# Optimization experiments

Hardware: AMD Instinct MI355X
Metric: run time of the kernel (lower is better)

## Reference

```python
import jax, jax.numpy as jnp
import numpy as np

IN_C = 256
OUT_C = 256
QK_C = OUT_C // 8  # channel_reduction_rate = 8
B, H, W = 8, 64, 64


def setup_inputs() -> dict:
    key = jax.random.key(0)
    ks = jax.random.split(key, 7)
    s_in = 1.0 / np.sqrt(IN_C)  # torch Conv2d default init scale (kernel=1)
    return {
        "x": jax.random.normal(ks[0], (B, IN_C, H, W), dtype=jnp.float32),
        "W1": jax.random.uniform(ks[1], (OUT_C, IN_C), jnp.float32, -s_in, s_in),
        "b1": jax.random.uniform(ks[2], (OUT_C,), jnp.float32, -s_in, s_in),
        "W2": jax.random.uniform(ks[3], (QK_C, IN_C), jnp.float32, -s_in, s_in),
        "b2": jax.random.uniform(ks[4], (QK_C,), jnp.float32, -s_in, s_in),
        "W3": jax.random.uniform(ks[5], (QK_C, IN_C), jnp.float32, -s_in, s_in),
        "b3": jax.random.uniform(ks[6], (QK_C,), jnp.float32, -s_in, s_in),
    }


def reference(x, W1, b1, W2, b2, W3, b3):
    b, c, h, w = x.shape
    n = h * w
    xf = x.reshape(b, c, n)  # 1x1 conv == channel matmul on flattened spatial
    v = jnp.einsum("oc,bcn->bon", W1, xf) + b1[None, :, None]   # [B, OUT_C, N]
    q = jnp.einsum("oc,bcn->bon", W2, xf) + b2[None, :, None]   # [B, QK_C, N]
    k = jnp.einsum("oc,bcn->bon", W3, xf) + b3[None, :, None]   # [B, QK_C, N]
    scores = jnp.einsum("bdn,bdm->bnm", q, k)                    # [B, N, N]
    # GLOBAL softmax over the full flattened NxN matrix per batch element
    attn = jax.nn.softmax(scores.reshape(b, -1), axis=1).reshape(b, n, n)
    out = jnp.einsum("bon,bnm->bom", v, attn)                    # [B, OUT_C, N]
    return out.reshape(x.shape) + x
```

## Files before the change

### kernel.cpp

```cpp
#include <hip/hip_runtime.h>
#include <hip/hip_bf16.h>
#include <math.h>

#define NBATCH 8
#define NC 256
#define ND 32
#define SN 4096

constexpr size_t VB_B   = 0;
constexpr size_t QT_B   = 16777216;
constexpr size_t KT_B   = QT_B + 2097152;
constexpr size_t PM_B   = KT_B + 2097152;
constexpr size_t PS_B   = PM_B + 32768;
constexpr size_t C_B    = PS_B + 32768;
constexpr size_t WB_B   = C_B + 64;
constexpr size_t BIAS_B = WB_B + 163840;
constexpr size_t PB_B   = BIAS_B + 1280;

typedef __attribute__((ext_vector_type(8))) short short8;
typedef __attribute__((ext_vector_type(4))) float f32x4;

__device__ __forceinline__ unsigned bf16rne(float f) {
  unsigned u = __float_as_uint(f);
  return (u + 0x7fffu + ((u >> 16) & 1u)) >> 16;
}
__device__ __forceinline__ unsigned bfpack2(float lo, float hi) {
  union { __hip_bfloat162 h; unsigned u; } cv;
  cv.h.x = __float2bfloat16(lo);
  cv.h.y = __float2bfloat16(hi);
  return cv.u;
}

__global__ __launch_bounds__(256) void prep_kernel(
    const float* __restrict__ W1, const float* __restrict__ b1,
    const float* __restrict__ W2, const float* __restrict__ b2,
    const float* __restrict__ W3, const float* __restrict__ b3,
    char* __restrict__ wsb)
{
  ushort* Wb = (ushort*)(wsb + WB_B);
  float* bias = (float*)(wsb + BIAS_B);
  const float LOG2E = 1.4426950408889634f;
  int idx = blockIdx.x * 256 + threadIdx.x;
  int r = idx >> 6, c4 = (idx & 63) * 4;
  float4 v; float sc = 1.0f;
  if (r < 256)      { v = *(const float4*)(W1 + (size_t)r * 256 + c4); }
  else if (r < 288) { v = *(const float4*)(W2 + (size_t)(r - 256) * 256 + c4); sc = LOG2E; }
  else              { v = *(const float4*)(W3 + (size_t)(r - 288) * 256 + c4); }
  ushort4 o;
  o.x = (ushort)bf16rne(v.x * sc); o.y = (ushort)bf16rne(v.y * sc);
  o.z = (ushort)bf16rne(v.z * sc); o.w = (ushort)bf16rne(v.w * sc);
  *(ushort4*)(Wb + (size_t)r * 256 + c4) = o;
  if (blockIdx.x == 0 && threadIdx.x < 320) {
    int q = threadIdx.x;
    bias[q] = q < 256 ? b1[q] : (q < 288 ? b2[q - 256] * LOG2E : b3[q - 288]);
  }
}

__global__ __launch_bounds__(512) void proj_kernel(
    const float* __restrict__ x, char* __restrict__ wsb)
{
  __shared__ alignas(16) char xT[65536];
  __shared__ alignas(16) char Wsh[40960];
  const int bid = blockIdx.x;
  const int b = bid & 7, nt = bid >> 3;
  const int n0 = nt * 128;
  const int t = threadIdx.x, w = t >> 6, lane = t & 63;
  const int l4 = lane >> 4, l16 = lane & 15;
  const float* xb = x + (size_t)b * NC * SN;
  const ushort* Wb = (const ushort*)(wsb + WB_B);
  const float* bias = (const float*)(wsb + BIAS_B);
  ushort* vbuf  = (ushort*)(wsb + VB_B);
  ushort* qtbuf = (ushort*)(wsb + QT_B);
  ushort* ktbuf = (ushort*)(wsb + KT_B);

  {
    int cp = w * 16 + l16;
    int c  = cp * 2;
    int nb0 = l4 * 4;
#pragma unroll
    for (int ni = 0; ni < 8; ++ni) {
      int nB = ni * 16 + nb0;
      float4 a0 = *(const float4*)(xb + (size_t)c * SN + n0 + nB);
      float4 a1 = *(const float4*)(xb + (size_t)(c + 1) * SN + n0 + nB);
      const float* p0 = (const float*)&a0;
      const float* p1 = (const float*)&a1;
#pragma unroll
      for (int j = 0; j < 4; ++j) {
        int n = nB + j;
        *(uint*)(xT + n * 512 + ((cp * 4) ^ ((n & 7) << 4))) = bfpack2(p0[j], p1[j]);
      }
    }
  }
#pragma unroll
  for (int ii = 0; ii < 5; ++ii) {
    int slot = t + ii * 512;
    int r = slot >> 3, cc = slot & 7;
    *(uint4*)(Wsh + r * 128 + ((cc * 16) ^ ((r & 7) << 4))) =
        *(const uint4*)(Wb + (size_t)r * 256 + cc * 8);
  }
  __syncthreads();

  const int of_g = w >> 1;
  const int nf_g = w & 1;
  f32x4 acc[5][4] = {};

  for (int c4 = 0; c4 < 4; ++c4) {
#pragma unroll
    for (int kk = 0; kk < 2; ++kk) {
      short8 a[4];
#pragma unroll
      for (int nf = 0; nf < 4; ++nf) {
        int n = nf_g * 64 + nf * 16 + l16;
        a[nf] = *(const short8*)(xT + n * 512 +
                 ((c4 * 128 + kk * 64 + l4 * 16) ^ ((n & 7) << 4)));
      }
#pragma unroll
      for (int of = 0; of < 5; ++of) {
        int o = (of_g * 5 + of) * 16 + l16;
        short8 bf = *(const short8*)(Wsh + o * 128 +
                    ((kk * 64 + l4 * 16) ^ ((o & 7) << 4)));
#pragma unroll
        for (int nf = 0; nf < 4; ++nf)
          acc[of][nf] = __builtin_amdgcn_mfma_f32_16x16x32_bf16(a[nf], bf, acc[of][nf], 0, 0, 0);
      }
    }
    if (c4 < 3) {
      __syncthreads();
#pragma unroll
      for (int ii = 0; ii < 5; ++ii) {
        int slot = t + ii * 512;
        int r = slot >> 3, cc = slot & 7;
        *(uint4*)(Wsh + r * 128 + ((cc * 16) ^ ((r & 7) << 4))) =
            *(const uint4*)(Wb + (size_t)r * 256 + (c4 + 1) * 64 + cc * 8);
      }
      __syncthreads();
    }
  }

#pragma unroll
  for (int of = 0; of < 5; ++of) {
    int o = (of_g * 5 + of) * 16 + l16;
    float bv = bias[o];
#pragma unroll
    for (int nf = 0; nf < 4; ++nf) {
      int nb = nf_g * 64 + nf * 16 + l4 * 4;
      float v0 = acc[of][nf][0] + bv, v1 = acc[of][nf][1] + bv;
      float v2 = acc[of][nf][2] + bv, v3 = acc[of][nf][3] + bv;
      if (o < 256) {
        uint2 pk; pk.x = bfpack2(v0, v1); pk.y = bfpack2(v2, v3);
        *(uint2*)(vbuf + ((size_t)b * NC + o) * SN + n0 + nb) = pk;
      } else if (o < 288) {
        int d = o - 256;
        qtbuf[((size_t)b * SN + n0 + nb + 0) * ND + d] = (ushort)bf16rne(v0);
        qtbuf[((size_t)b * SN + n0 + nb + 1) * ND + d] = (ushort)bf16rne(v1);
        qtbuf[((size_t)b * SN + n0 + nb + 2) * ND + d] = (ushort)bf16rne(v2);
        qtbuf[((size_t)b * SN + n0 + nb + 3) * ND + d] = (ushort)bf16rne(v3);
      } else {
        int d = o - 288;
        ktbuf[((size_t)b * SN + n0 + nb + 0) * ND + d] = (ushort)bf16rne(v0);
        ktbuf[((size_t)b * SN + n0 + nb + 1) * ND + d] = (ushort)bf16rne(v1);
        ktbuf[((size_t)b * SN + n0 + nb + 2) * ND + d] = (ushort)bf16rne(v2);
        ktbuf[((size_t)b * SN + n0 + nb + 3) * ND + d] = (ushort)bf16rne(v3);
      }
    }
  }
}

__global__ __launch_bounds__(256) void qk_stats(
    const char* __restrict__ wsb, float* __restrict__ pm, float* __restrict__ ps)
{
  __shared__ alignas(16) char qt_s[128 * 64];
  __shared__ alignas(16) char kt_s[128 * 64];
  __shared__ float wm[4], wz[4];
  const int bid = blockIdx.x;
  const int b = bid & 7, ny = (bid >> 3) & 31, mx = bid >> 8;
  const int n0 = ny * 128, m0 = mx * 128;
  const int t = threadIdx.x, w = t >> 6, lane = t & 63;
  const int l4 = lane >> 4, l16 = lane & 15;
  const ushort* qtb = (const ushort*)(wsb + QT_B) + (size_t)b * SN * ND;
  const ushort* ktb = (const ushort*)(wsb + KT_B) + (size_t)b * SN * ND;
  {
    int row = t >> 1, db = (t & 1) * 32;
#pragma unroll
    for (int i = 0; i < 2; ++i) {
      int b16 = db + i * 16;
      int dst = row * 64 + (b16 ^ ((row & 3) << 4));
      *(uint4*)(qt_s + dst) = *(const uint4*)(qtb + (size_t)(n0 + row) * ND + b16 / 2);
      *(uint4*)(kt_s + dst) = *(const uint4*)(ktb + (size_t)(m0 + row) * ND + b16 / 2);
    }
  }
  __syncthreads();
  const f32x4 zf = {0.f, 0.f, 0.f, 0.f};
  short8 bfr[2];
#pragma unroll
  for (int j = 0; j < 2; ++j) {
    int mm = (w * 2 + j) * 16 + l16;
    bfr[j] = *(const short8*)(kt_s + mm * 64 + ((l4 * 16) ^ ((mm & 3) << 4)));
  }
  f32x4 sfr[8][2];
#pragma unroll
  for (int i = 0; i < 8; ++i) {
    int nn = i * 16 + l16;
    short8 af = *(const short8*)(qt_s + nn * 64 + ((l4 * 16) ^ ((nn & 3) << 4)));
#pragma unroll
    for (int j = 0; j < 2; ++j)
      sfr[i][j] = __builtin_amdgcn_mfma_f32_16x16x32_bf16(af, bfr[j], zf, 0, 0, 0);
  }
  float mt = -1e30f;
#pragma unroll
  for (int i = 0; i < 8; ++i)
#pragma unroll
    for (int j = 0; j < 2; ++j)
#pragma unroll
      for (int r = 0; r < 4; ++r) mt = fmaxf(mt, sfr[i][j][r]);
  float zt = 0.f;
#pragma unroll
  for (int i = 0; i < 8; ++i)
#pragma unroll
    for (int j = 0; j < 2; ++j)
#pragma unroll
      for (int r = 0; r < 4; ++r) zt += exp2f(sfr[i][j][r] - mt);

#pragma unroll
  for (int off = 1; off < 64; off <<= 1) {
    float m2 = __shfl_xor(mt, off);
    float z2 = __shfl_xor(zt, off);
    float M = fmaxf(mt, m2);
    zt = zt * exp2f(mt - M) + z2 * exp2f(m2 - M);
    mt = M;
  }
  if (lane == 0) { wm[w] = mt; wz[w] = zt; }
  __syncthreads();
  if (t == 0) {
    float m = wm[0], z = wz[0];
#pragma unroll
    for (int i = 1; i < 4; ++i) {
      float M = fmaxf(m, wm[i]);
      z = z * exp2f(m - M) + wz[i] * exp2f(wm[i] - M);
      m = M;
    }
    int idx = (b * 32 + ny) * 32 + mx;
    pm[idx] = m; ps[idx] = z;
  }
}

__global__ __launch_bounds__(256) void reduce_kernel(char* __restrict__ wsb)
{
  const int b = blockIdx.x;
  const float* pm = (const float*)(wsb + PM_B) + (size_t)b * 1024;
  const float* ps = (const float*)(wsb + PS_B) + (size_t)b * 1024;
  const int t = threadIdx.x;
  float m = -1e30f, z = 0.f;
  for (int i = t; i < 1024; i += 256) {
    float m2 = pm[i], z2 = ps[i];
    float M = fmaxf(m, m2);
    z = z * exp2f(m - M) + z2 * exp2f(m2 - M);
    m = M;
  }
#pragma unroll
  for (int off = 1; off < 64; off <<= 1) {
    float m2 = __shfl_xor(m, off);
    float z2 = __shfl_xor(z, off);
    float M = fmaxf(m, m2);
    z = z * exp2f(m - M) + z2 * exp2f(m2 - M);
    m = M;
  }
  __shared__ float wm[4], wz[4];
  int w = t >> 6;
  if ((t & 63) == 0) { wm[w] = m; wz[w] = z; }
  __syncthreads();
  if (t == 0) {
    float M = wm[0], Z = wz[0];
#pragma unroll
    for (int i = 1; i < 4; ++i) {
      float Mn = fmaxf(M, wm[i]);
      Z = Z * exp2f(M - Mn) + wz[i] * exp2f(wm[i] - Mn);
      M = Mn;
    }
    ((float*)(wsb + C_B))[b] = M + log2f(Z);
  }
}

__global__ __launch_bounds__(512, 4) void attn_out(
    char* __restrict__ wsb, float* __restrict__ out)
{
  __shared__ alignas(16) char qt_s[2][8192];
  __shared__ alignas(16) char as_s[2][16384];
  const int bid = blockIdx.x;
  const int b = bid & 7;
  const int rest = bid >> 3;
  const int mt = rest & 63;
  const int half = rest >> 6;
  const int m0 = mt * 64;
  const int nbase = half * 2048;
  const int t = threadIdx.x, w = t >> 6, lane = t & 63;
  const int l4 = lane >> 4, l16 = lane & 15;
  const ushort* vb  = (const ushort*)(wsb + VB_B) + (size_t)b * NC * SN;
  const ushort* qtb = (const ushort*)(wsb + QT_B) + (size_t)b * SN * ND;
  const ushort* ktb = (const ushort*)(wsb + KT_B) + (size_t)b * SN * ND;
  const float Cb = ((const float*)(wsb + C_B))[b];

  const int mfS = w & 3;
  const int nh  = w >> 2;
  const int mS_l = mfS * 16 + l16;
  short8 bfr = *(const short8*)(ktb + (size_t)(m0 + mS_l) * ND + l4 * 8);

  const int as_wb = mfS * 1024 + l16 * 16 + (l4 & 1) * 8;
  const int l4h = l4 >> 1;

  const int qrow = t >> 2, qsl = t & 3;
  const int qt_addr = (qrow >> 4) * 1024 + ((qsl * 16 + (qrow & 15)) << 4);

  const ushort* vrow0 = vb + (size_t)(w * 32 + l16) * SN + nbase + l4 * 8;
  const ushort* vrow1 = vrow0 + (size_t)16 * SN;

  const f32x4 zf = {0.f, 0.f, 0.f, 0.f};
  f32x4 acc[2][4] = {};

  *(uint4*)(qt_s[0] + qt_addr) = *(const uint4*)(qtb + (size_t)(nbase + qrow) * ND + qsl * 8);
  __syncthreads();

  for (int i = 0; i < 16; ++i) {
    const int cur = i & 1;
    short8 vf[2][4];
#pragma unroll
    for (int kk = 0; kk < 4; ++kk) {
      vf[0][kk] = *(const short8*)(vrow0 + i * 128 + kk * 32);
      vf[1][kk] = *(const short8*)(vrow1 + i * 128 + kk * 32);
    }
    uint4 qnext;
    const bool pf = (i < 15);
    if (pf) qnext = *(const uint4*)(qtb + (size_t)(nbase + (i + 1) * 128 + qrow) * ND + qsl * 8);

#pragma unroll
    for (int ii = 0; ii < 4; ++ii) {
      int nf = nh * 4 + ii;
      short8 af = *(const short8*)(qt_s[cur] + nf * 1024 + lane * 16);
      f32x4 sv = __builtin_amdgcn_mfma_f32_16x16x32_bf16(af, bfr, zf, 0, 0, 0);
      uint2 pk;
      pk.x = bfpack2(exp2f(sv[0] - Cb), exp2f(sv[1] - Cb));
      pk.y = bfpack2(exp2f(sv[2] - Cb), exp2f(sv[3] - Cb));
      int addr = (nf >> 1) * 4096 + ((nf * 2 + l4h) & 3) * 256 + as_wb;
      *(uint2*)(as_s[cur] + addr) = pk;
    }
    if (pf)
      *(uint4*)(qt_s[cur ^ 1] + qt_addr) = qnext;
    __syncthreads();

    __builtin_amdgcn_s_setprio(1);
#pragma unroll
    for (int kk = 0; kk < 4; ++kk) {
#pragma unroll
      for (int mf = 0; mf < 4; ++mf) {
        short8 paf = *(const short8*)(as_s[cur] + (kk * 4 + mf) * 1024 + lane * 16);
        acc[0][mf] = __builtin_amdgcn_mfma_f32_16x16x32_bf16(vf[0][kk], paf, acc[0][mf], 0, 0, 0);
        acc[1][mf] = __builtin_amdgcn_mfma_f32_16x16x32_bf16(vf[1][kk], paf, acc[1][mf], 0, 0, 0);
      }
    }
    __builtin_amdgcn_s_setprio(0);
  }

  if (half == 0) {
    ushort* pb = (ushort*)(wsb + PB_B);
#pragma unroll
    for (int of = 0; of < 2; ++of)
#pragma unroll
      for (int mf = 0; mf < 4; ++mf) {
        int m = m0 + mf * 16 + l16;
#pragma unroll
        for (int j = 0; j < 4; ++j) {
          int o = w * 32 + of * 16 + l4 * 4 + j;
          pb[((size_t)b * NC + o) * SN + m] = (ushort)bf16rne(acc[of][mf][j]);
        }
      }
  } else {
#pragma unroll
    for (int of = 0; of < 2; ++of)
#pragma unroll
      for (int mf = 0; mf < 4; ++mf) {
        int m = m0 + mf * 16 + l16;
#pragma unroll
        for (int j = 0; j < 4; ++j) {
          int o = w * 32 + of * 16 + l4 * 4 + j;
          out[((size_t)b * NC + o) * SN + m] = acc[of][mf][j];
        }
      }
  }
}

__global__ __launch_bounds__(256) void combine_kernel(
    const char* __restrict__ wsb, const float* __restrict__ x, float* __restrict__ out)
{
  const ushort* pb = (const ushort*)(wsb + PB_B);
  const size_t total = (size_t)NBATCH * NC * SN;
  for (size_t i = ((size_t)blockIdx.x * 256 + threadIdx.x) * 4; i < total;
       i += (size_t)gridDim.x * 256 * 4) {
    float4 o = *(const float4*)(out + i);
    ushort4 p = *(const ushort4*)(pb + i);
    float4 xx = *(const float4*)(x + i);
    o.x += __uint_as_float((unsigned)p.x << 16) + xx.x;
    o.y += __uint_as_float((unsigned)p.y << 16) + xx.y;
    o.z += __uint_as_float((unsigned)p.z << 16) + xx.z;
    o.w += __uint_as_float((unsigned)p.w << 16) + xx.w;
    *(float4*)(out + i) = o;
  }
}

extern "C" void kernel_launch(void* const* d_in, const int* in_sizes, int n_in,
                              void* d_out, int out_size, void* d_ws, size_t ws_size,
                              hipStream_t stream)
{
  const float* x  = (const float*)d_in[0];
  const float* W1 = (const float*)d_in[1];
  const float* b1 = (const float*)d_in[2];
  const float* W2 = (const float*)d_in[3];
  const float* b2 = (const float*)d_in[4];
  const float* W3 = (const float*)d_in[5];
  const float* b3 = (const float*)d_in[6];
  char* wsb  = (char*)d_ws;
  float* out = (float*)d_out;

  prep_kernel<<<80, 256, 0, stream>>>(W1, b1, W2, b2, W3, b3, wsb);
  proj_kernel<<<256, 512, 0, stream>>>(x, wsb);
  qk_stats<<<8192, 256, 0, stream>>>(wsb, (float*)(wsb + PM_B), (float*)(wsb + PS_B));
  reduce_kernel<<<NBATCH, 256, 0, stream>>>(wsb);
  attn_out<<<1024, 512, 0, stream>>>(wsb, out);
  combine_kernel<<<2048, 256, 0, stream>>>(wsb, x, out);
}
```

Before: 224.5 us.

## Shrink attn_out blocks to 4 waves with 64 output channels per wave

Halves attn_out workgroups from 512 to 256 threads. Each wave now owns 64 output channels (4 MFMA row fragments) rather than 32, and processes 64-row n-chunks over 32 iterations. Each wave computes one score fragment per n-subtile, so score/exp work is no longer duplicated across wave halves, and each P fragment read from LDS feeds four MFMAs instead of two. The -Cb offset is folded into the MFMA accumulator init, removing the subtractions before exp2. The cost is more accumulator registers, twice as many barriers, and smaller blocks, which may lower occupancy or latency hiding.

Result: no change. 221.5 us (-1.4%).

```diff
diff --git a/kernel.cpp b/kernel.cpp
--- a/kernel.cpp
+++ b/kernel.cpp
@@ -281,11 +281,11 @@
   }
 }
 
-__global__ __launch_bounds__(512, 4) void attn_out(
+__global__ __launch_bounds__(256, 4) void attn_out(
     char* __restrict__ wsb, float* __restrict__ out)
 {
-  __shared__ alignas(16) char qt_s[2][8192];
-  __shared__ alignas(16) char as_s[2][16384];
+  __shared__ alignas(16) char qt_s[2][4096];
+  __shared__ alignas(16) char as_s[2][8192];
   const int bid = blockIdx.x;
   const int b = bid & 7;
   const int rest = bid >> 3;
@@ -300,47 +300,42 @@
   const ushort* ktb = (const ushort*)(wsb + KT_B) + (size_t)b * SN * ND;
   const float Cb = ((const float*)(wsb + C_B))[b];
 
-  const int mfS = w & 3;
-  const int nh  = w >> 2;
-  const int mS_l = mfS * 16 + l16;
-  short8 bfr = *(const short8*)(ktb + (size_t)(m0 + mS_l) * ND + l4 * 8);
-
-  const int as_wb = mfS * 1024 + l16 * 16 + (l4 & 1) * 8;
+  short8 bfr = *(const short8*)(ktb + (size_t)(m0 + w * 16 + l16) * ND + l4 * 8);
+  const f32x4 cinit = {-Cb, -Cb, -Cb, -Cb};
+
+  const int as_wb = w * 1024 + l16 * 16 + (l4 & 1) * 8;
   const int l4h = l4 >> 1;
 
-  const int qrow = t >> 2, qsl = t & 3;
-  const int qt_addr = (qrow >> 4) * 1024 + ((qsl * 16 + (qrow & 15)) << 4);
-
-  const ushort* vrow0 = vb + (size_t)(w * 32 + l16) * SN + nbase + l4 * 8;
-  const ushort* vrow1 = vrow0 + (size_t)16 * SN;
-
-  const f32x4 zf = {0.f, 0.f, 0.f, 0.f};
-  f32x4 acc[2][4] = {};
-
-  *(uint4*)(qt_s[0] + qt_addr) = *(const uint4*)(qtb + (size_t)(nbase + qrow) * ND + qsl * 8);
+  const int qrow = w * 16 + l16;
+  const int qt_addr = w * 1024 + lane * 16;
+
+  const ushort* vrow = vb + (size_t)(w * 64 + l16) * SN + nbase + l4 * 8;
+
+  f32x4 acc[4][4] = {};
+
+  *(uint4*)(qt_s[0] + qt_addr) = *(const uint4*)(qtb + (size_t)(nbase + qrow) * ND + l4 * 8);
   __syncthreads();
 
-  for (int i = 0; i < 16; ++i) {
+  for (int i = 0; i < 32; ++i) {
     const int cur = i & 1;
     short8 vf[2][4];
 #pragma unroll
-    for (int kk = 0; kk < 4; ++kk) {
-      vf[0][kk] = *(const short8*)(vrow0 + i * 128 + kk * 32);
-      vf[1][kk] = *(const short8*)(vrow1 + i * 128 + kk * 32);
-    }
+    for (int kk = 0; kk < 2; ++kk)
+#pragma unroll
+      for (int of = 0; of < 4; ++of)
+        vf[kk][of] = *(const short8*)(vrow + (size_t)(of * 16) * SN + i * 64 + kk * 32);
     uint4 qnext;
-    const bool pf = (i < 15);
-    if (pf) qnext = *(const uint4*)(qtb + (size_t)(nbase + (i + 1) * 128 + qrow) * ND + qsl * 8);
-
-#pragma unroll
-    for (int ii = 0; ii < 4; ++ii) {
-      int nf = nh * 4 + ii;
+    const bool pf = (i < 31);
+    if (pf) qnext = *(const uint4*)(qtb + (size_t)(nbase + (i + 1) * 64 + qrow) * ND + l4 * 8);
+
+#pragma unroll
+    for (int nf = 0; nf < 4; ++nf) {
       short8 af = *(const short8*)(qt_s[cur] + nf * 1024 + lane * 16);
-      f32x4 sv = __builtin_amdgcn_mfma_f32_16x16x32_bf16(af, bfr, zf, 0, 0, 0);
+      f32x4 sv = __builtin_amdgcn_mfma_f32_16x16x32_bf16(af, bfr, cinit, 0, 0, 0);
       uint2 pk;
-      pk.x = bfpack2(exp2f(sv[0] - Cb), exp2f(sv[1] - Cb));
-      pk.y = bfpack2(exp2f(sv[2] - Cb), exp2f(sv[3] - Cb));
-      int addr = (nf >> 1) * 4096 + ((nf * 2 + l4h) & 3) * 256 + as_wb;
+      pk.x = bfpack2(exp2f(sv[0]), exp2f(sv[1]));
+      pk.y = bfpack2(exp2f(sv[2]), exp2f(sv[3]));
+      int addr = (nf >> 1) * 4096 + (((nf & 1) * 2 + l4h) & 3) * 256 + as_wb;
       *(uint2*)(as_s[cur] + addr) = pk;
     }
     if (pf)
@@ -349,12 +344,13 @@
 
     __builtin_amdgcn_s_setprio(1);
 #pragma unroll
-    for (int kk = 0; kk < 4; ++kk) {
+    for (int kk = 0; kk < 2; ++kk) {
 #pragma unroll
       for (int mf = 0; mf < 4; ++mf) {
         short8 paf = *(const short8*)(as_s[cur] + (kk * 4 + mf) * 1024 + lane * 16);
-        acc[0][mf] = __builtin_amdgcn_mfma_f32_16x16x32_bf16(vf[0][kk], paf, acc[0][mf], 0, 0, 0);
-        acc[1][mf] = __builtin_amdgcn_mfma_f32_16x16x32_bf16(vf[1][kk], paf, acc[1][mf], 0, 0, 0);
+#pragma unroll
+        for (int of = 0; of < 4; ++of)
+          acc[of][mf] = __builtin_amdgcn_mfma_f32_16x16x32_bf16(vf[kk][of], paf, acc[of][mf], 0, 0, 0);
       }
     }
     __builtin_amdgcn_s_setprio(0);
@@ -363,25 +359,25 @@
   if (half == 0) {
     ushort* pb = (ushort*)(wsb + PB_B);
 #pragma unroll
-    for (int of = 0; of < 2; ++of)
+    for (int of = 0; of < 4; ++of)
 #pragma unroll
       for (int mf = 0; mf < 4; ++mf) {
         int m = m0 + mf * 16 + l16;
 #pragma unroll
         for (int j = 0; j < 4; ++j) {
-          int o = w * 32 + of * 16 + l4 * 4 + j;
+          int o = w * 64 + of * 16 + l4 * 4 + j;
           pb[((size_t)b * NC + o) * SN + m] = (ushort)bf16rne(acc[of][mf][j]);
         }
       }
   } else {
 #pragma unroll
-    for (int of = 0; of < 2; ++of)
+    for (int of = 0; of < 4; ++of)
 #pragma unroll
       for (int mf = 0; mf < 4; ++mf) {
         int m = m0 + mf * 16 + l16;
 #pragma unroll
         for (int j = 0; j < 4; ++j) {
-          int o = w * 32 + of * 16 + l4 * 4 + j;
+          int o = w * 64 + of * 16 + l4 * 4 + j;
           out[((size_t)b * NC + o) * SN + m] = acc[of][mf][j];
         }
       }
@@ -424,6 +420,6 @@
   proj_kernel<<<256, 512, 0, stream>>>(x, wsb);
   qk_stats<<<8192, 256, 0, stream>>>(wsb, (float*)(wsb + PM_B), (float*)(wsb + PS_B));
   reduce_kernel<<<NBATCH, 256, 0, stream>>>(wsb);
-  attn_out<<<1024, 512, 0, stream>>>(wsb, out);
+  attn_out<<<1024, 256, 0, stream>>>(wsb, out);
   combine_kernel<<<2048, 256, 0, stream>>>(wsb, x, out);
 }
```
